# Kernel optimization log

Hardware: AMD Instinct MI355X
Metric: run time of the kernel (lower is better)

The kernel has to match this reference:

```python
import jax, jax.numpy as jnp
import numpy as np

S, B, D = 2048, 8, 2048


def setup_inputs() -> dict:
    key = jax.random.key(0)
    ks = jax.random.split(key, 10)
    scale = 1.0 / np.sqrt(D)
    return {
        "x": jax.random.normal(ks[0], (S, B, D), dtype=jnp.float32),
        "layer_input": jax.random.normal(ks[1], (S, B, D), dtype=jnp.float32),
        "position_embedding": jax.random.normal(ks[2], (S, B, D), dtype=jnp.float32),
        "encoder_padding_mask": jnp.zeros((B, S), dtype=bool),
        "langs": jnp.zeros((B,), dtype=jnp.int64),
        "W1": jax.random.uniform(ks[3], (D, D), jnp.float32, -scale, scale),
        "b1": jax.random.uniform(ks[4], (D,), jnp.float32, -scale, scale),
        "W2": jax.random.uniform(ks[5], (D, D), jnp.float32, -scale, scale),
        "b2": jax.random.uniform(ks[6], (D,), jnp.float32, -scale, scale),
        "V": jax.random.uniform(ks[7], (D, D), jnp.float32, -scale, scale),
        "bV": jax.random.uniform(ks[8], (D,), jnp.float32, -scale, scale),
    }


def reference(x, layer_input, position_embedding, encoder_padding_mask, langs,
              W1, b1, W2, b2, V, bV):
    # Uniform-language path of LSReorderingLayer -> ReorderingLayer (LA_reorder=False).
    # x, layer_input, position_embedding: (S, B, D)
    # position_penalty = tanh(W1(layer_input) + W2(x))
    pp = jnp.tanh(jnp.einsum('sbd,ed->sbe', layer_input, W1) + b1
                  + jnp.einsum('sbd,ed->sbe', x, W2) + b2)
    # position_penalty = sigmoid(V(pp)); reordering = penalty * position_embedding
    gate = jax.nn.sigmoid(jnp.einsum('sbd,ed->sbe', pp, V) + bV)
    return gate * position_embedding
```

## Files before the change

kernel.cpp:

```cpp
#include <hip/hip_runtime.h>
#include <hip/hip_bf16.h>
#include <cstdint>
#include <cstddef>

typedef unsigned short u16;
typedef short short8 __attribute__((ext_vector_type(8)));
typedef float floatx4 __attribute__((ext_vector_type(4)));

#define BM 128
#define BN 128
#define BK 32
#define D_DIM 2048

__device__ __forceinline__ void async_ld16(const u16* g, u16* l) {
  __builtin_amdgcn_global_load_lds(
      (const __attribute__((address_space(1))) void*)g,
      (__attribute__((address_space(3))) void*)l, 16, 0, 0);
}

__device__ __forceinline__ u16 f2bf(float f) {
  __hip_bfloat16 h = __float2bfloat16(f);
  return *reinterpret_cast<u16*>(&h);
}

__device__ __forceinline__ short8 pack8(float4 a, float4 b) {
  short8 p;
  p[0] = (short)f2bf(a.x); p[1] = (short)f2bf(a.y);
  p[2] = (short)f2bf(a.z); p[3] = (short)f2bf(a.w);
  p[4] = (short)f2bf(b.x); p[5] = (short)f2bf(b.y);
  p[6] = (short)f2bf(b.z); p[7] = (short)f2bf(b.w);
  return p;
}

__global__ __launch_bounds__(256) void cvt_f32_bf16(
    const float* __restrict__ src, u16* __restrict__ dst, int n8) {
  int i = blockIdx.x * blockDim.x + threadIdx.x;
  if (i < n8) {
    const float4* s = (const float4*)src + 2 * (size_t)i;
    float4 f0 = s[0], f1 = s[1];
    *((short8*)dst + i) = pack8(f0, f1);
  }
}

__device__ __forceinline__ void phase_bf16(
    const u16* __restrict__ A, const u16* __restrict__ Bw,
    int mBase, int nBase, u16* As, u16* Bs, floatx4 acc[4][4])
{
  const int tid  = threadIdx.x;
  const int lane = tid & 63;
  const int quad = lane >> 4;
  const int lrow = lane & 15;
  const int wv   = tid >> 6;
  const int wm   = wv & 1;
  const int wn   = wv >> 1;

  const int r0 = tid >> 2;
  const int q0 = (((tid & 3) ^ ((tid >> 3) & 3))) * 8;
  const u16* gA = A + (size_t)(mBase + r0) * D_DIM + q0;
  const u16* gB = Bw + (size_t)(nBase + r0) * D_DIM + q0;
  u16* lA0 = As + tid * 8;
  u16* lA1 = As + (tid + 256) * 8;
  u16* lB0 = Bs + tid * 8;
  u16* lB1 = Bs + (tid + 256) * 8;

  const int slot8 = (quad ^ ((lrow >> 1) & 3)) * 8;

  for (int kt = 0; kt < D_DIM / BK; ++kt) {
    const int k0 = kt * BK;
    __syncthreads();
    async_ld16(gA + k0, lA0);
    async_ld16(gA + (size_t)64 * D_DIM + k0, lA1);
    async_ld16(gB + k0, lB0);
    async_ld16(gB + (size_t)64 * D_DIM + k0, lB1);
    __syncthreads();

    short8 a[4], b[4];
#pragma unroll
    for (int i = 0; i < 4; ++i) {
      const int row = wm * 64 + i * 16 + lrow;
      a[i] = *(const short8*)(As + row * BK + slot8);
      const int col = wn * 64 + i * 16 + lrow;
      b[i] = *(const short8*)(Bs + col * BK + slot8);
    }
#pragma unroll
    for (int i = 0; i < 4; ++i)
#pragma unroll
      for (int j = 0; j < 4; ++j)
        acc[i][j] = __builtin_amdgcn_mfma_f32_16x16x32_bf16(a[i], b[j], acc[i][j], 0, 0, 0);
  }
}

__device__ __forceinline__ void phase_f32A(
    const float* __restrict__ A, const u16* __restrict__ Bw,
    int mBase, int nBase, u16* As, u16* Bs, floatx4 acc[4][4])
{
  const int tid  = threadIdx.x;
  const int lane = tid & 63;
  const int quad = lane >> 4;
  const int lrow = lane & 15;
  const int wv   = tid >> 6;
  const int wm   = wv & 1;
  const int wn   = wv >> 1;

  const int r0 = tid >> 2;
  const int c0 = (tid & 3) * 8;
  const u16* gB = Bw + (size_t)(nBase + r0) * D_DIM + c0;
  u16* lB0 = Bs + tid * 8;
  u16* lB1 = Bs + (tid + 256) * 8;

  const int ar = tid >> 1;
  const int ac = (tid & 1) * 16;
  const float* gA = A + (size_t)(mBase + ar) * D_DIM + ac;
  u16* wA = As + ar * BK + ac;

  for (int kt = 0; kt < D_DIM / BK; ++kt) {
    const int k0 = kt * BK;
    __syncthreads();
    async_ld16(gB + k0, lB0);
    async_ld16(gB + (size_t)64 * D_DIM + k0, lB1);
    float4 f0 = *(const float4*)(gA + k0);
    float4 f1 = *(const float4*)(gA + k0 + 4);
    float4 f2 = *(const float4*)(gA + k0 + 8);
    float4 f3 = *(const float4*)(gA + k0 + 12);
    *(short8*)(wA)     = pack8(f0, f1);
    *(short8*)(wA + 8) = pack8(f2, f3);
    __syncthreads();

    short8 a[4], b[4];
#pragma unroll
    for (int i = 0; i < 4; ++i) {
      const int row = wm * 64 + i * 16 + lrow;
      a[i] = *(const short8*)(As + row * BK + quad * 8);
      const int col = wn * 64 + i * 16 + lrow;
      b[i] = *(const short8*)(Bs + col * BK + quad * 8);
    }
#pragma unroll
    for (int i = 0; i < 4; ++i)
#pragma unroll
      for (int j = 0; j < 4; ++j)
        acc[i][j] = __builtin_amdgcn_mfma_f32_16x16x32_bf16(a[i], b[j], acc[i][j], 0, 0, 0);
  }
}

__device__ __forceinline__ void epilogue_pp(
    floatx4 acc[4][4], const float* b1, const float* b2,
    int mBase, int nBase, u16* pp)
{
  const int tid  = threadIdx.x;
  const int lane = tid & 63;
  const int quad = lane >> 4;
  const int lrow = lane & 15;
  const int wv   = tid >> 6;
  const int wm   = wv & 1;
  const int wn   = wv >> 1;

#pragma unroll
  for (int j = 0; j < 4; ++j) {
    const int col = nBase + wn * 64 + j * 16 + lrow;
    const float bs = b1[col] + b2[col];
#pragma unroll
    for (int i = 0; i < 4; ++i) {
      const int rowb = mBase + wm * 64 + i * 16 + quad * 4;
#pragma unroll
      for (int r = 0; r < 4; ++r) {
        const float v = tanhf(acc[i][j][r] + bs);
        pp[(size_t)(rowb + r) * D_DIM + col] = f2bf(v);
      }
    }
  }
}

__global__ __launch_bounds__(256) void gemm_pp_bf16(
    const u16* __restrict__ lib, const u16* __restrict__ xb,
    const u16* __restrict__ w1b, const u16* __restrict__ w2b,
    const float* __restrict__ b1, const float* __restrict__ b2,
    u16* __restrict__ pp)
{
  __shared__ __align__(16) u16 As[BM * BK];
  __shared__ __align__(16) u16 Bs[BN * BK];

  floatx4 acc[4][4];
#pragma unroll
  for (int i = 0; i < 4; ++i)
#pragma unroll
    for (int j = 0; j < 4; ++j)
      acc[i][j] = (floatx4){0.f, 0.f, 0.f, 0.f};

  const int nBase = blockIdx.x * BN;
  const int mBase = blockIdx.y * BM;

  phase_bf16(lib, w1b, mBase, nBase, As, Bs, acc);
  phase_bf16(xb,  w2b, mBase, nBase, As, Bs, acc);
  epilogue_pp(acc, b1, b2, mBase, nBase, pp);
}

__global__ __launch_bounds__(256) void gemm_pp_f32(
    const float* __restrict__ li, const float* __restrict__ x,
    const u16* __restrict__ w1b, const u16* __restrict__ w2b,
    const float* __restrict__ b1, const float* __restrict__ b2,
    u16* __restrict__ pp)
{
  __shared__ __align__(16) u16 As[BM * BK];
  __shared__ __align__(16) u16 Bs[BN * BK];

  floatx4 acc[4][4];
#pragma unroll
  for (int i = 0; i < 4; ++i)
#pragma unroll
    for (int j = 0; j < 4; ++j)
      acc[i][j] = (floatx4){0.f, 0.f, 0.f, 0.f};

  const int nBase = blockIdx.x * BN;
  const int mBase = blockIdx.y * BM;

  phase_f32A(li, w1b, mBase, nBase, As, Bs, acc);
  phase_f32A(x,  w2b, mBase, nBase, As, Bs, acc);
  epilogue_pp(acc, b1, b2, mBase, nBase, pp);
}

__global__ __launch_bounds__(256) void gemm_out_kernel(
    const u16* __restrict__ pp, const u16* __restrict__ vb,
    const float* __restrict__ bV, const float* __restrict__ pe,
    float* __restrict__ out)
{
  __shared__ __align__(16) u16 As[BM * BK];
  __shared__ __align__(16) u16 Bs[BN * BK];

  floatx4 acc[4][4];
#pragma unroll
  for (int i = 0; i < 4; ++i)
#pragma unroll
    for (int j = 0; j < 4; ++j)
      acc[i][j] = (floatx4){0.f, 0.f, 0.f, 0.f};

  const int nBase = blockIdx.x * BN;
  const int mBase = blockIdx.y * BM;

  phase_bf16(pp, vb, mBase, nBase, As, Bs, acc);

  const int tid  = threadIdx.x;
  const int lane = tid & 63;
  const int quad = lane >> 4;
  const int lrow = lane & 15;
  const int wv   = tid >> 6;
  const int wm   = wv & 1;
  const int wn   = wv >> 1;

#pragma unroll
  for (int j = 0; j < 4; ++j) {
    const int col = nBase + wn * 64 + j * 16 + lrow;
    const float bs = bV[col];
#pragma unroll
    for (int i = 0; i < 4; ++i) {
      const int rowb = mBase + wm * 64 + i * 16 + quad * 4;
#pragma unroll
      for (int r = 0; r < 4; ++r) {
        const size_t idx = (size_t)(rowb + r) * D_DIM + col;
        const float t = acc[i][j][r] + bs;
        const float g = 1.f / (1.f + expf(-t));
        out[idx] = g * pe[idx];
      }
    }
  }
}

extern "C" void kernel_launch(void* const* d_in, const int* in_sizes, int n_in,
                              void* d_out, int out_size, void* d_ws, size_t ws_size,
                              hipStream_t stream) {
  const float* x  = (const float*)d_in[0];
  const float* li = (const float*)d_in[1];
  const float* pe = (const float*)d_in[2];
  const float* W1 = (const float*)d_in[5];
  const float* b1 = (const float*)d_in[6];
  const float* W2 = (const float*)d_in[7];
  const float* b2 = (const float*)d_in[8];
  const float* V  = (const float*)d_in[9];
  const float* bV = (const float*)d_in[10];
  float* out = (float*)d_out;

  const int M = 2048 * 8;
  const size_t nW  = (size_t)D_DIM * D_DIM;
  const size_t nA  = (size_t)M * D_DIM;

  u16* w1b = (u16*)d_ws;
  u16* w2b = w1b + nW;
  u16* vb  = w2b + nW;
  u16* pp  = vb  + nW;
  u16* lib = pp  + nA;
  u16* xb  = lib + nA;
  const size_t need_full = (3 * nW + 3 * nA) * sizeof(u16);

  const int nW8 = (int)(nW / 8);
  const int nA8 = (int)(nA / 8);

  cvt_f32_bf16<<<nW8 / 256, 256, 0, stream>>>(W1, w1b, nW8);
  cvt_f32_bf16<<<nW8 / 256, 256, 0, stream>>>(W2, w2b, nW8);
  cvt_f32_bf16<<<nW8 / 256, 256, 0, stream>>>(V,  vb,  nW8);

  dim3 grid(D_DIM / BN, M / BM);
  dim3 block(256);

  if (ws_size >= need_full) {
    cvt_f32_bf16<<<nA8 / 256, 256, 0, stream>>>(li, lib, nA8);
    cvt_f32_bf16<<<nA8 / 256, 256, 0, stream>>>(x,  xb,  nA8);
    gemm_pp_bf16<<<grid, block, 0, stream>>>(lib, xb, w1b, w2b, b1, b2, pp);
  } else {
    gemm_pp_f32<<<grid, block, 0, stream>>>(li, x, w1b, w2b, b1, b2, pp);
  }
  gemm_out_kernel<<<grid, block, 0, stream>>>(pp, vb, bV, pe, out);
}
```

Measured before the change: 1.053 ms.

## Replace GEMM kernels with 256x256 eight-wave pipelined double-buffered MFMA GEMM

Replaces the 128x128 single-buffered GEMM kernels with a 256x256-tile, 512-thread kernel. It double-buffers K tiles in 128KB of LDS, issuing async global-to-LDS loads interleaved with MFMA phases under barriers and s_setprio. Both GEMMs use a swizzled block order for L2 reuse, and the epilogues switch to fast exp-based tanh and sigmoid. This aims to hide memory latency and raise MFMA utilization. The trade-offs are heavy register and LDS pressure, fragile hand-tuned waitcnt logic, and slightly less accurate activation functions.

```diff
diff --git a/kernel.cpp b/kernel.cpp
--- a/kernel.cpp
+++ b/kernel.cpp
@@ -7,10 +7,10 @@
 typedef short short8 __attribute__((ext_vector_type(8)));
 typedef float floatx4 __attribute__((ext_vector_type(4)));
 
+#define D_DIM 2048
 #define BM 128
 #define BN 128
 #define BK 32
-#define D_DIM 2048
 
 __device__ __forceinline__ void async_ld16(const u16* g, u16* l) {
   __builtin_amdgcn_global_load_lds(
@@ -30,6 +30,14 @@
   p[4] = (short)f2bf(b.x); p[5] = (short)f2bf(b.y);
   p[6] = (short)f2bf(b.z); p[7] = (short)f2bf(b.w);
   return p;
+}
+
+__device__ __forceinline__ float fast_tanh(float x) {
+  const float e = __expf(2.f * x);
+  return 1.f - 2.f / (e + 1.f);
+}
+__device__ __forceinline__ float fast_sigmoid(float x) {
+  return 1.f / (1.f + __expf(-x));
 }
 
 __global__ __launch_bounds__(256) void cvt_f32_bf16(
@@ -42,9 +50,11 @@
   }
 }
 
-__device__ __forceinline__ void phase_bf16(
-    const u16* __restrict__ A, const u16* __restrict__ Bw,
-    int mBase, int nBase, u16* As, u16* Bs, floatx4 acc[4][4])
+template <int NT>
+__device__ __forceinline__ void gemm256_8ph(
+    const u16* __restrict__ A0, const u16* __restrict__ A1,
+    const u16* __restrict__ B0, const u16* __restrict__ B1,
+    int mBase, int nBase, u16* lds, floatx4 (&acc)[2][4][2][2])
 {
   const int tid  = threadIdx.x;
   const int lane = tid & 63;
@@ -54,40 +64,247 @@
   const int wm   = wv & 1;
   const int wn   = wv >> 1;
 
-  const int r0 = tid >> 2;
-  const int q0 = (((tid & 3) ^ ((tid >> 3) & 3))) * 8;
-  const u16* gA = A + (size_t)(mBase + r0) * D_DIM + q0;
-  const u16* gB = Bw + (size_t)(nBase + r0) * D_DIM + q0;
-  u16* lA0 = As + tid * 8;
-  u16* lA1 = As + (tid + 256) * 8;
-  u16* lB0 = Bs + tid * 8;
-  u16* lB1 = Bs + (tid + 256) * 8;
-
-  const int slot8 = (quad ^ ((lrow >> 1) & 3)) * 8;
-
-  for (int kt = 0; kt < D_DIM / BK; ++kt) {
-    const int k0 = kt * BK;
-    __syncthreads();
-    async_ld16(gA + k0, lA0);
-    async_ld16(gA + (size_t)64 * D_DIM + k0, lA1);
-    async_ld16(gB + k0, lB0);
-    async_ld16(gB + (size_t)64 * D_DIM + k0, lB1);
-    __syncthreads();
-
-    short8 a[4], b[4];
-#pragma unroll
-    for (int i = 0; i < 4; ++i) {
-      const int row = wm * 64 + i * 16 + lrow;
-      a[i] = *(const short8*)(As + row * BK + slot8);
-      const int col = wn * 64 + i * 16 + lrow;
-      b[i] = *(const short8*)(Bs + col * BK + slot8);
-    }
-#pragma unroll
-    for (int i = 0; i < 4; ++i)
-#pragma unroll
-      for (int j = 0; j < 4; ++j)
-        acc[i][j] = __builtin_amdgcn_mfma_f32_16x16x32_bf16(a[i], b[j], acc[i][j], 0, 0, 0);
+  const int lr0   = (tid >> 2) & 15;
+  const int rowc0 = ((tid >> 7) << 4) + lr0;
+  const int kc0   = (((tid >> 6) & 1) << 5)
+                  + (((tid & 3) ^ ((lr0 >> 3) << 1)) << 3);
+  const size_t aOff = (size_t)(mBase + rowc0) * D_DIM + kc0;
+  const size_t bOff = (size_t)(nBase + rowc0) * D_DIM + kc0;
+  u16* const dst0 = lds + tid * 8;
+
+  auto stage_half = [&](int j) {
+    const int T = j >> 2, slot = j & 3;
+    const int h = slot & 1, msel = slot >> 1;
+    const u16* pA = (T & 32) ? A1 : A0;
+    const u16* pB = (T & 32) ? B1 : B0;
+    const u16* src = (msel ? (pB + bOff) : (pA + aOff))
+                   + (size_t)(h * 128) * D_DIM + ((T & 31) << 6);
+    u16* dst = dst0 + ((T & 1) << 15) + (msel << 14) + (h << 13);
+    async_ld16(src, dst);
+    async_ld16(src + (size_t)64 * D_DIM, dst + 4096);
+  };
+
+  const int rdoff = (lrow << 5) + ((quad << 3) ^ ((lrow >> 3) << 4));
+  const u16* const rdA = lds + rdoff + (wm << 12);
+  const u16* const rdB = lds + 16384 + rdoff + (wn << 11);
+
+  short8 a[4][2];
+  short8 b[2][2][2];
+
+  const int J = 4 * NT;
+
+#pragma unroll
+  for (int j = 0; j < 7; ++j) stage_half(j);
+  asm volatile("s_waitcnt vmcnt(6)" ::: "memory");
+  __builtin_amdgcn_s_barrier();
+
+#pragma unroll 2
+  for (int t = 0; t < NT; ++t) {
+    const u16* rA = rdA + ((t & 1) << 15);
+    const u16* rB = rdB + ((t & 1) << 15);
+
+#pragma unroll
+    for (int m = 0; m < 4; ++m)
+#pragma unroll
+      for (int ks = 0; ks < 2; ++ks)
+        a[m][ks] = *(const short8*)(rA + (m << 10) + (ks << 9));
+#pragma unroll
+    for (int n = 0; n < 2; ++n)
+#pragma unroll
+      for (int ks = 0; ks < 2; ++ks)
+        b[0][n][ks] = *(const short8*)(rB + (n << 10) + (ks << 9));
+    if (4 * t + 7 < J) stage_half(4 * t + 7);
+    __builtin_amdgcn_s_barrier();
+    asm volatile("s_waitcnt lgkmcnt(0)" ::: "memory");
+    __builtin_amdgcn_s_setprio(1);
+#pragma unroll
+    for (int m = 0; m < 4; ++m)
+#pragma unroll
+      for (int n = 0; n < 2; ++n)
+#pragma unroll
+        for (int ks = 0; ks < 2; ++ks)
+          acc[0][m][0][n] = __builtin_amdgcn_mfma_f32_16x16x32_bf16(
+              a[m][ks], b[0][n][ks], acc[0][m][0][n], 0, 0, 0);
+    __builtin_amdgcn_s_setprio(0);
+    __builtin_amdgcn_s_barrier();
+
+#pragma unroll
+    for (int n = 0; n < 2; ++n)
+#pragma unroll
+      for (int ks = 0; ks < 2; ++ks)
+        b[1][n][ks] = *(const short8*)(rB + 8192 + (n << 10) + (ks << 9));
+    if (4 * t + 8 < J) stage_half(4 * t + 8);
+    __builtin_amdgcn_s_barrier();
+    asm volatile("s_waitcnt lgkmcnt(0)" ::: "memory");
+    __builtin_amdgcn_s_setprio(1);
+#pragma unroll
+    for (int m = 0; m < 4; ++m)
+#pragma unroll
+      for (int n = 0; n < 2; ++n)
+#pragma unroll
+        for (int ks = 0; ks < 2; ++ks)
+          acc[0][m][1][n] = __builtin_amdgcn_mfma_f32_16x16x32_bf16(
+              a[m][ks], b[1][n][ks], acc[0][m][1][n], 0, 0, 0);
+    __builtin_amdgcn_s_setprio(0);
+    __builtin_amdgcn_s_barrier();
+
+#pragma unroll
+    for (int m = 0; m < 4; ++m)
+#pragma unroll
+      for (int ks = 0; ks < 2; ++ks)
+        a[m][ks] = *(const short8*)(rA + 8192 + (m << 10) + (ks << 9));
+    if (4 * t + 10 < J) stage_half(4 * t + 10);
+    __builtin_amdgcn_s_barrier();
+    asm volatile("s_waitcnt lgkmcnt(0)" ::: "memory");
+    __builtin_amdgcn_s_setprio(1);
+#pragma unroll
+    for (int m = 0; m < 4; ++m)
+#pragma unroll
+      for (int n = 0; n < 2; ++n)
+#pragma unroll
+        for (int ks = 0; ks < 2; ++ks)
+          acc[1][m][1][n] = __builtin_amdgcn_mfma_f32_16x16x32_bf16(
+              a[m][ks], b[1][n][ks], acc[1][m][1][n], 0, 0, 0);
+    __builtin_amdgcn_s_setprio(0);
+    __builtin_amdgcn_s_barrier();
+
+    if (4 * t + 9 < J) stage_half(4 * t + 9);
+    __builtin_amdgcn_s_barrier();
+    asm volatile("s_waitcnt lgkmcnt(0)" ::: "memory");
+    __builtin_amdgcn_s_setprio(1);
+#pragma unroll
+    for (int m = 0; m < 4; ++m)
+#pragma unroll
+      for (int n = 0; n < 2; ++n)
+#pragma unroll
+        for (int ks = 0; ks < 2; ++ks)
+          acc[1][m][0][n] = __builtin_amdgcn_mfma_f32_16x16x32_bf16(
+              a[m][ks], b[0][n][ks], acc[1][m][0][n], 0, 0, 0);
+    __builtin_amdgcn_s_setprio(0);
+    if (t < NT - 2) {
+      asm volatile("s_waitcnt vmcnt(6)" ::: "memory");
+    } else if (t == NT - 2) {
+      asm volatile("s_waitcnt vmcnt(0)" ::: "memory");
+    }
+    __builtin_amdgcn_s_barrier();
   }
+}
+
+__global__ __launch_bounds__(512, 2) void gemm_pp_8ph(
+    const u16* __restrict__ lib, const u16* __restrict__ xb,
+    const u16* __restrict__ w1b, const u16* __restrict__ w2b,
+    const float* __restrict__ b1, const float* __restrict__ b2,
+    u16* __restrict__ pp)
+{
+  __shared__ __align__(16) u16 lds[65536];
+  const int bid = blockIdx.x;
+  const int swz = (bid & 7) * 64 + (bid >> 3);
+  const int mBase = (swz >> 3) << 8;
+  const int nBase = (swz & 7) << 8;
+
+  floatx4 acc[2][4][2][2];
+#pragma unroll
+  for (int mh = 0; mh < 2; ++mh)
+#pragma unroll
+    for (int m = 0; m < 4; ++m)
+#pragma unroll
+      for (int nh = 0; nh < 2; ++nh)
+#pragma unroll
+        for (int n = 0; n < 2; ++n)
+          acc[mh][m][nh][n] = (floatx4){0.f, 0.f, 0.f, 0.f};
+
+  gemm256_8ph<64>(lib, xb, w1b, w2b, mBase, nBase, lds, acc);
+
+  const int tid  = threadIdx.x;
+  const int lane = tid & 63;
+  const int quad = lane >> 4;
+  const int lrow = lane & 15;
+  const int wm   = (tid >> 6) & 1;
+  const int wn   = tid >> 7;
+
+  float bsum[2][2];
+#pragma unroll
+  for (int nh = 0; nh < 2; ++nh)
+#pragma unroll
+    for (int n = 0; n < 2; ++n) {
+      const int col = nBase + nh * 128 + wn * 32 + n * 16 + lrow;
+      bsum[nh][n] = b1[col] + b2[col];
+    }
+#pragma unroll
+  for (int mh = 0; mh < 2; ++mh)
+#pragma unroll
+    for (int m = 0; m < 4; ++m) {
+      const int rowb = mBase + mh * 128 + wm * 64 + m * 16 + quad * 4;
+#pragma unroll
+      for (int nh = 0; nh < 2; ++nh)
+#pragma unroll
+        for (int n = 0; n < 2; ++n) {
+          const int col = nBase + nh * 128 + wn * 32 + n * 16 + lrow;
+#pragma unroll
+          for (int r = 0; r < 4; ++r) {
+            const float v = fast_tanh(acc[mh][m][nh][n][r] + bsum[nh][n]);
+            pp[(size_t)(rowb + r) * D_DIM + col] = f2bf(v);
+          }
+        }
+    }
+}
+
+__global__ __launch_bounds__(512, 2) void gemm_out_8ph(
+    const u16* __restrict__ pp, const u16* __restrict__ vb,
+    const float* __restrict__ bV, const float* __restrict__ pe,
+    float* __restrict__ out)
+{
+  __shared__ __align__(16) u16 lds[65536];
+  const int bid = blockIdx.x;
+  const int swz = (bid & 7) * 64 + (bid >> 3);
+  const int mBase = (swz >> 3) << 8;
+  const int nBase = (swz & 7) << 8;
+
+  floatx4 acc[2][4][2][2];
+#pragma unroll
+  for (int mh = 0; mh < 2; ++mh)
+#pragma unroll
+    for (int m = 0; m < 4; ++m)
+#pragma unroll
+      for (int nh = 0; nh < 2; ++nh)
+#pragma unroll
+        for (int n = 0; n < 2; ++n)
+          acc[mh][m][nh][n] = (floatx4){0.f, 0.f, 0.f, 0.f};
+
+  gemm256_8ph<32>(pp, pp, vb, vb, mBase, nBase, lds, acc);
+
+  const int tid  = threadIdx.x;
+  const int lane = tid & 63;
+  const int quad = lane >> 4;
+  const int lrow = lane & 15;
+  const int wm   = (tid >> 6) & 1;
+  const int wn   = tid >> 7;
+
+  float bsv[2][2];
+#pragma unroll
+  for (int nh = 0; nh < 2; ++nh)
+#pragma unroll
+    for (int n = 0; n < 2; ++n) {
+      const int col = nBase + nh * 128 + wn * 32 + n * 16 + lrow;
+      bsv[nh][n] = bV[col];
+    }
+#pragma unroll
+  for (int mh = 0; mh < 2; ++mh)
+#pragma unroll
+    for (int m = 0; m < 4; ++m) {
+      const int rowb = mBase + mh * 128 + wm * 64 + m * 16 + quad * 4;
+#pragma unroll
+      for (int nh = 0; nh < 2; ++nh)
+#pragma unroll
+        for (int n = 0; n < 2; ++n) {
+          const int col = nBase + nh * 128 + wn * 32 + n * 16 + lrow;
+#pragma unroll
+          for (int r = 0; r < 4; ++r) {
+            const size_t idx = (size_t)(rowb + r) * D_DIM + col;
+            out[idx] = fast_sigmoid(acc[mh][m][nh][n][r] + bsv[nh][n]) * pe[idx];
+          }
+        }
+    }
 }
 
 __device__ __forceinline__ void phase_f32A(
@@ -142,58 +359,6 @@
   }
 }
 
-__device__ __forceinline__ void epilogue_pp(
-    floatx4 acc[4][4], const float* b1, const float* b2,
-    int mBase, int nBase, u16* pp)
-{
-  const int tid  = threadIdx.x;
-  const int lane = tid & 63;
-  const int quad = lane >> 4;
-  const int lrow = lane & 15;
-  const int wv   = tid >> 6;
-  const int wm   = wv & 1;
-  const int wn   = wv >> 1;
-
-#pragma unroll
-  for (int j = 0; j < 4; ++j) {
-    const int col = nBase + wn * 64 + j * 16 + lrow;
-    const float bs = b1[col] + b2[col];
-#pragma unroll
-    for (int i = 0; i < 4; ++i) {
-      const int rowb = mBase + wm * 64 + i * 16 + quad * 4;
-#pragma unroll
-      for (int r = 0; r < 4; ++r) {
-        const float v = tanhf(acc[i][j][r] + bs);
-        pp[(size_t)(rowb + r) * D_DIM + col] = f2bf(v);
-      }
-    }
-  }
-}
-
-__global__ __launch_bounds__(256) void gemm_pp_bf16(
-    const u16* __restrict__ lib, const u16* __restrict__ xb,
-    const u16* __restrict__ w1b, const u16* __restrict__ w2b,
-    const float* __restrict__ b1, const float* __restrict__ b2,
-    u16* __restrict__ pp)
-{
-  __shared__ __align__(16) u16 As[BM * BK];
-  __shared__ __align__(16) u16 Bs[BN * BK];
-
-  floatx4 acc[4][4];
-#pragma unroll
-  for (int i = 0; i < 4; ++i)
-#pragma unroll
-    for (int j = 0; j < 4; ++j)
-      acc[i][j] = (floatx4){0.f, 0.f, 0.f, 0.f};
-
-  const int nBase = blockIdx.x * BN;
-  const int mBase = blockIdx.y * BM;
-
-  phase_bf16(lib, w1b, mBase, nBase, As, Bs, acc);
-  phase_bf16(xb,  w2b, mBase, nBase, As, Bs, acc);
-  epilogue_pp(acc, b1, b2, mBase, nBase, pp);
-}
-
 __global__ __launch_bounds__(256) void gemm_pp_f32(
     const float* __restrict__ li, const float* __restrict__ x,
     const u16* __restrict__ w1b, const u16* __restrict__ w2b,
@@ -215,28 +380,6 @@
 
   phase_f32A(li, w1b, mBase, nBase, As, Bs, acc);
   phase_f32A(x,  w2b, mBase, nBase, As, Bs, acc);
-  epilogue_pp(acc, b1, b2, mBase, nBase, pp);
-}
-
-__global__ __launch_bounds__(256) void gemm_out_kernel(
-    const u16* __restrict__ pp, const u16* __restrict__ vb,
-    const float* __restrict__ bV, const float* __restrict__ pe,
-    float* __restrict__ out)
-{
-  __shared__ __align__(16) u16 As[BM * BK];
-  __shared__ __align__(16) u16 Bs[BN * BK];
-
-  floatx4 acc[4][4];
-#pragma unroll
-  for (int i = 0; i < 4; ++i)
-#pragma unroll
-    for (int j = 0; j < 4; ++j)
-      acc[i][j] = (floatx4){0.f, 0.f, 0.f, 0.f};
-
-  const int nBase = blockIdx.x * BN;
-  const int mBase = blockIdx.y * BM;
-
-  phase_bf16(pp, vb, mBase, nBase, As, Bs, acc);
 
   const int tid  = threadIdx.x;
   const int lane = tid & 63;
@@ -249,16 +392,14 @@
 #pragma unroll
   for (int j = 0; j < 4; ++j) {
     const int col = nBase + wn * 64 + j * 16 + lrow;
-    const float bs = bV[col];
+    const float bs = b1[col] + b2[col];
 #pragma unroll
     for (int i = 0; i < 4; ++i) {
       const int rowb = mBase + wm * 64 + i * 16 + quad * 4;
 #pragma unroll
       for (int r = 0; r < 4; ++r) {
-        const size_t idx = (size_t)(rowb + r) * D_DIM + col;
-        const float t = acc[i][j][r] + bs;
-        const float g = 1.f / (1.f + expf(-t));
-        out[idx] = g * pe[idx];
+        const float v = fast_tanh(acc[i][j][r] + bs);
+        pp[(size_t)(rowb + r) * D_DIM + col] = f2bf(v);
       }
     }
   }
@@ -297,15 +438,13 @@
   cvt_f32_bf16<<<nW8 / 256, 256, 0, stream>>>(W2, w2b, nW8);
   cvt_f32_bf16<<<nW8 / 256, 256, 0, stream>>>(V,  vb,  nW8);
 
-  dim3 grid(D_DIM / BN, M / BM);
-  dim3 block(256);
-
   if (ws_size >= need_full) {
     cvt_f32_bf16<<<nA8 / 256, 256, 0, stream>>>(li, lib, nA8);
     cvt_f32_bf16<<<nA8 / 256, 256, 0, stream>>>(x,  xb,  nA8);
-    gemm_pp_bf16<<<grid, block, 0, stream>>>(lib, xb, w1b, w2b, b1, b2, pp);
+    gemm_pp_8ph<<<dim3(512), dim3(512), 0, stream>>>(lib, xb, w1b, w2b, b1, b2, pp);
   } else {
-    gemm_pp_f32<<<grid, block, 0, stream>>>(li, x, w1b, w2b, b1, b2, pp);
+    dim3 grid(D_DIM / BN, M / BM);
+    gemm_pp_f32<<<grid, dim3(256), 0, stream>>>(li, x, w1b, w2b, b1, b2, pp);
   }
-  gemm_out_kernel<<<grid, block, 0, stream>>>(pp, vb, bV, pe, out);
-}
+  gemm_out_8ph<<<dim3(512), dim3(512), 0, stream>>>(pp, vb, bV, pe, out);
+}
```

Result: no change. 1.036 ms (-1.6%).
